# Performance work log

Hardware: AMD Instinct MI355X
Metric: run time of the kernel (lower is better)

## Reference

```python
import jax, jax.numpy as jnp
import numpy as np

B, C, H, W = 8, 128, 64, 64
C8, C2 = C // 8, C // 2


def conv1x1(x, w, b):
    # x: [B,Cin,H,W], w: [Cout,Cin], b: [Cout]
    return jnp.einsum('bchw,oc->bohw', x, w) + b[None, :, None, None]


def maxpool2(x):
    # 2x2 stride-2 max pool on [B,C,H,W]
    b, c, h, w = x.shape
    return x.reshape(b, c, h // 2, 2, w // 2, 2).max(axis=(3, 5))


def setup_inputs() -> dict:
    key = jax.random.key(0)
    ks = jax.random.split(key, 10)
    s_in = 1.0 / np.sqrt(C)
    s_c2 = 1.0 / np.sqrt(C2)
    return {
        'x': jax.random.normal(ks[0], (B, C, H, W), dtype=jnp.float32),
        'w_theta': jax.random.uniform(ks[1], (C8, C), jnp.float32, -s_in, s_in),
        'b_theta': jax.random.uniform(ks[2], (C8,), jnp.float32, -s_in, s_in),
        'w_phi': jax.random.uniform(ks[3], (C8, C), jnp.float32, -s_in, s_in),
        'b_phi': jax.random.uniform(ks[4], (C8,), jnp.float32, -s_in, s_in),
        'w_g': jax.random.uniform(ks[5], (C2, C), jnp.float32, -s_in, s_in),
        'b_g': jax.random.uniform(ks[6], (C2,), jnp.float32, -s_in, s_in),
        'w_attn': jax.random.uniform(ks[7], (C, C2), jnp.float32, -s_c2, s_c2),
        'b_attn': jax.random.uniform(ks[8], (C,), jnp.float32, -s_c2, s_c2),
        'sigma': jnp.zeros((1,), dtype=jnp.float32),
    }


def reference(x, w_theta, b_theta, w_phi, b_phi, w_g, b_g, w_attn, b_attn, sigma):
    b, ch, h, w = x.shape
    n, m = h * w, (h * w) // 4
    theta = conv1x1(x, w_theta, b_theta).reshape(b, ch // 8, n)          # [B,C8,N]
    phi = maxpool2(conv1x1(x, w_phi, b_phi)).reshape(b, ch // 8, m)      # [B,C8,M]
    attn = jax.nn.softmax(jnp.einsum('bdn,bdm->bnm', theta, phi), axis=-1)  # [B,N,M]
    g = maxpool2(conv1x1(x, w_g, b_g)).reshape(b, ch // 2, m)            # [B,C2,M]
    attn_g = jnp.einsum('bcm,bnm->bcn', g, attn).reshape(b, ch // 2, h, w)
    attn_g = conv1x1(attn_g, w_attn, b_attn)
    return x + sigma[0] * attn_g
```

## Files before the change

kernel.cpp:

```cpp
#include <hip/hip_runtime.h>
#include <math.h>

#define Bn 8
#define Cn 128
#define Nn 4096
#define Mn 1024
#define C8n 16
#define C2n 64

typedef __attribute__((ext_vector_type(8))) short short8;
typedef __attribute__((ext_vector_type(4))) float floatx4;
typedef __attribute__((ext_vector_type(4))) unsigned short ushortx4;

__device__ __forceinline__ unsigned short f2bf(float f) {
    union { float f; unsigned u; } v; v.f = f;
    unsigned r = v.u + 0x7fff + ((v.u >> 16) & 1);
    return (unsigned short)(r >> 16);
}

__global__ __launch_bounds__(256) void k1_pre(
    const float* __restrict__ x,
    const float* __restrict__ w_theta, const float* __restrict__ b_theta,
    const float* __restrict__ w_phi,   const float* __restrict__ b_phi,
    const float* __restrict__ w_g,     const float* __restrict__ b_g,
    unsigned short* __restrict__ thA,
    unsigned short* __restrict__ phB,
    unsigned short* __restrict__ gB)
{
    __shared__ unsigned short wA[6 * 4 * 64 * 8];
    __shared__ unsigned short xB[8 * 4 * 64 * 8];
    __shared__ unsigned short pool[80][33];
    __shared__ float biases[96];

    const int t    = threadIdx.x;
    const int b    = blockIdx.x & 7;
    const int h2   = blockIdx.x >> 3;
    const int wv   = t >> 6;
    const int lane = t & 63;
    const int q    = lane >> 4;
    const int l15  = lane & 15;
    const float L2E = 1.4426950408889634f;

    if (t < 96)
        biases[t] = (t < 16) ? b_theta[t] * L2E
                  : (t < 32) ? b_phi[t - 16] : b_g[t - 32];

    #pragma unroll
    for (int k = 0; k < 12; ++k) {
        int u  = t + k * 256;
        int oc = u >> 5, c4 = u & 31;
        const float* src = (oc < 16) ? (w_theta + oc * Cn)
                         : (oc < 32) ? (w_phi + (oc - 16) * Cn)
                                     : (w_g + (oc - 32) * Cn);
        float4 wv4 = *(const float4*)(src + c4 * 4);
        float sc = (oc < 16) ? L2E : 1.f;
        int c = c4 * 4;
        int ot = oc >> 4, kc = c >> 5, qq = (c >> 3) & 3, jj = c & 7;
        ushortx4 pk = { f2bf(wv4.x * sc), f2bf(wv4.y * sc),
                        f2bf(wv4.z * sc), f2bf(wv4.w * sc) };
        *(ushortx4*)(wA + (((ot * 4 + kc) * 64 + qq * 16 + (oc & 15)) * 8 + jj)) = pk;
    }

    const float* xb = x + (size_t)b * Cn * Nn + h2 * 128;
    #pragma unroll
    for (int k = 0; k < 16; ++k) {
        int u   = t + k * 256;
        int pos = u & 127, c4 = u >> 7;
        int c   = c4 * 4;
        float v0 = xb[(size_t)(c + 0) * Nn + pos];
        float v1 = xb[(size_t)(c + 1) * Nn + pos];
        float v2 = xb[(size_t)(c + 2) * Nn + pos];
        float v3 = xb[(size_t)(c + 3) * Nn + pos];
        int pt = pos >> 4, kc = c >> 5, qq = (c >> 3) & 3, jj = c & 7;
        ushortx4 pk = { f2bf(v0), f2bf(v1), f2bf(v2), f2bf(v3) };
        *(ushortx4*)(xB + (((pt * 4 + kc) * 64 + qq * 16 + (pos & 15)) * 8 + jj)) = pk;
    }
    __syncthreads();

    floatx4 acc[6][2];
    #pragma unroll
    for (int ot = 0; ot < 6; ++ot)
        #pragma unroll
        for (int p2 = 0; p2 < 2; ++p2) acc[ot][p2] = (floatx4){0.f, 0.f, 0.f, 0.f};

    #pragma unroll
    for (int kc = 0; kc < 4; ++kc) {
        short8 Bf0 = *(const short8*)(xB + ((wv * 4 + kc) * 64 + lane) * 8);
        short8 Bf1 = *(const short8*)(xB + (((wv + 4) * 4 + kc) * 64 + lane) * 8);
        #pragma unroll
        for (int ot = 0; ot < 6; ++ot) {
            short8 Af = *(const short8*)(wA + ((ot * 4 + kc) * 64 + lane) * 8);
            acc[ot][0] = __builtin_amdgcn_mfma_f32_16x16x32_bf16(Af, Bf0, acc[ot][0], 0, 0, 0);
            acc[ot][1] = __builtin_amdgcn_mfma_f32_16x16x32_bf16(Af, Bf1, acc[ot][1], 0, 0, 0);
        }
    }

    #pragma unroll
    for (int p2 = 0; p2 < 2; ++p2) {
        const int pt = wv + p2 * 4;
        ushortx4 pk;
        #pragma unroll
        for (int r = 0; r < 4; ++r)
            pk[r] = f2bf(acc[0][p2][r] + biases[q * 4 + r]);
        *(ushortx4*)(thA + ((((size_t)b * 256 + h2 * 8 + pt) * 2 + (q >> 1)) * 128
                            + l15 * 8 + (q & 1) * 4)) = pk;
    }

    #pragma unroll
    for (int ot = 1; ot < 6; ++ot) {
        #pragma unroll
        for (int r = 0; r < 4; ++r) {
            float vmax = fmaxf(acc[ot][0][r], acc[ot][1][r]);
            float pmax = fmaxf(vmax, __shfl_xor(vmax, 1, 64));
            if ((l15 & 1) == 0) {
                int oc = (ot - 1) * 16 + q * 4 + r;
                int w2 = wv * 8 + (l15 >> 1);
                pool[oc][w2] = f2bf(pmax + biases[16 + oc]);
            }
        }
    }
    __syncthreads();

    if (t < 64) {
        int w2h = t >> 5, ml = (t >> 1) & 15, dh = t & 1;
        int w2 = w2h * 16 + ml;
        ushortx4 lo, hi;
        #pragma unroll
        for (int j = 0; j < 4; ++j) { lo[j] = pool[dh * 8 + j][w2];
                                      hi[j] = pool[dh * 8 + 4 + j][w2]; }
        unsigned short* dst = phB + (((size_t)b * 64 + h2 * 2 + w2h) * 2 + dh) * 128 + ml * 8;
        *(ushortx4*)dst = lo;
        *(ushortx4*)(dst + 4) = hi;
    }
    {
        int c = t >> 2, sq = t & 3;
        ushortx4 lo, hi;
        #pragma unroll
        for (int j = 0; j < 8; ++j) {
            int w2 = (j & 1) * 16 + sq * 4 + (j >> 1);
            unsigned short v = pool[16 + c][w2];
            if (j < 4) lo[j] = v; else hi[j - 4] = v;
        }
        unsigned short* dst = gB + ((((size_t)b * 32 + h2) * 4 + (c >> 4)) * 4 + sq) * 128
                              + (c & 15) * 8;
        *(ushortx4*)dst = lo;
        *(ushortx4*)(dst + 4) = hi;
    }
}

__global__ __launch_bounds__(256, 2) void k2_attn(
    const float* __restrict__ x,
    const unsigned short* __restrict__ thA,
    const unsigned short* __restrict__ phB,
    const unsigned short* __restrict__ gB,
    const float* __restrict__ w_attn, const float* __restrict__ b_attn,
    const float* __restrict__ sigma_p,
    float* __restrict__ out)
{
    __shared__ float smem[18816];
    unsigned short* phis = (unsigned short*)smem;
    unsigned short* gs   = (unsigned short*)smem + 4096;
    char* Pall = (char*)smem + 40960;
    float* battn = (float*)((char*)smem + 74752);

    const int tid  = threadIdx.x;
    const int wave = tid >> 6;
    const int lane = tid & 63;
    const int q    = lane >> 4;
    const int l15  = lane & 15;
    const int b    = blockIdx.x & 7;
    const int n0   = (blockIdx.x >> 3) * 64;
    const int nw   = n0 + wave * 16;
    char* Pbase = Pall + wave * 8448;

    const float sg = sigma_p[0];

    short8 thf = {};
    if (q < 2)
        thf = *(const short8*)(thA + ((((size_t)b * 256 + (nw >> 4)) * 2 + q) * 16 + l15) * 8);

    floatx4 O[4];
    #pragma unroll
    for (int cs = 0; cs < 4; ++cs) O[cs] = (floatx4){0.f, 0.f, 0.f, 0.f};
    float L[4]    = {0.f, 0.f, 0.f, 0.f};
    float rmax[4] = {-1e30f, -1e30f, -1e30f, -1e30f};

    for (int s = 0; s < 4; ++s) {
        __syncthreads();
        {
            const float4* psrc = (const float4*)(phB + ((size_t)b * 64 + s * 16) * 256);
            const float4* gsrc = (const float4*)(gB + ((size_t)b * 32 + s * 8) * 2048);
            #pragma unroll
            for (int k = 0; k < 10; ++k) {
                int i = tid + k * 256;
                if (i < 512) ((float4*)smem)[i] = psrc[i];
                else ((float4*)((char*)smem + 8192))[i - 512] = gsrc[i - 512];
            }
        }
        __syncthreads();

        floatx4 S[16];
        #pragma unroll
        for (int mt = 0; mt < 16; ++mt) {
            short8 bf = {};
            if (q < 2) bf = *(const short8*)(phis + ((mt * 2 + q) * 16 + l15) * 8);
            S[mt] = __builtin_amdgcn_mfma_f32_16x16x32_bf16(
                        thf, bf, (floatx4){0.f, 0.f, 0.f, 0.f}, 0, 0, 0);
        }

        float cm[4];
        #pragma unroll
        for (int r = 0; r < 4; ++r) cm[r] = S[0][r];
        #pragma unroll
        for (int mt = 1; mt < 16; ++mt)
            #pragma unroll
            for (int r = 0; r < 4; ++r) cm[r] = fmaxf(cm[r], S[mt][r]);
        #pragma unroll
        for (int d = 1; d <= 8; d <<= 1)
            #pragma unroll
            for (int r = 0; r < 4; ++r) cm[r] = fmaxf(cm[r], __shfl_xor(cm[r], d, 64));
        float f[4];
        #pragma unroll
        for (int r = 0; r < 4; ++r) {
            float nm = fmaxf(rmax[r], cm[r]);
            f[r] = exp2f(rmax[r] - nm);
            rmax[r] = nm;
            L[r] *= f[r];
        }
        #pragma unroll
        for (int cs = 0; cs < 4; ++cs)
            #pragma unroll
            for (int r = 0; r < 4; ++r) O[cs][r] *= f[r];

        #pragma unroll
        for (int g2 = 0; g2 < 8; ++g2) {
            #pragma unroll
            for (int r = 0; r < 4; ++r) {
                float pa = exp2f(S[2 * g2][r]     - rmax[r]);
                float pb = exp2f(S[2 * g2 + 1][r] - rmax[r]);
                L[r] += pa + pb;
                unsigned dw = (unsigned)f2bf(pa) | ((unsigned)f2bf(pb) << 16);
                *(unsigned*)(Pbase + (q * 4 + r) * 528 + g2 * 64 + l15 * 4) = dw;
            }
        }
        __syncthreads();

        #pragma unroll
        for (int ch = 0; ch < 8; ++ch) {
            short8 Af = *(const short8*)(Pbase + l15 * 528 + ch * 64 + q * 16);
            const unsigned short* gchunk = gs + ch * 2048;
            #pragma unroll
            for (int cs = 0; cs < 4; ++cs) {
                short8 Bf = *(const short8*)(gchunk + ((cs * 4 + q) * 16 + l15) * 8);
                O[cs] = __builtin_amdgcn_mfma_f32_16x16x32_bf16(Af, Bf, O[cs], 0, 0, 0);
            }
        }
    }

    __syncthreads();
    {
        unsigned short* wAe = (unsigned short*)smem;
        #pragma unroll
        for (int k = 0; k < 8; ++k) {
            int i = tid + k * 256;
            float4 wv = ((const float4*)w_attn)[i];
            int o = i >> 4, c4 = (i & 15) * 4;
            float vv[4] = {wv.x, wv.y, wv.z, wv.w};
            #pragma unroll
            for (int j = 0; j < 4; ++j) {
                int c = c4 + j;
                wAe[((o >> 4) * 2 + (c >> 5)) * 512 + (o & 15) * 32 + (c & 31)] = f2bf(vv[j]);
            }
        }
        if (tid < 128) battn[tid] = b_attn[tid];
    }
    {
        float inv[4];
        #pragma unroll
        for (int r = 0; r < 4; ++r) inv[r] = 1.0f / L[r];
        unsigned short* Ob = (unsigned short*)Pbase;
        #pragma unroll
        for (int cs = 0; cs < 4; ++cs)
            #pragma unroll
            for (int r = 0; r < 4; ++r)
                Ob[(q * 4 + r) * 72 + cs * 16 + l15] = f2bf(O[cs][r] * inv[r]);
    }
    __syncthreads();

    {
        unsigned short* wAe = (unsigned short*)smem;
        unsigned short* Ob = (unsigned short*)Pbase;
        short8 B0 = *(const short8*)(Ob + l15 * 72 + q * 8);
        short8 B1 = *(const short8*)(Ob + l15 * 72 + 32 + q * 8);
        const float* xw = x   + (size_t)b * Cn * Nn + nw + l15;
        float*       ow = out + (size_t)b * Cn * Nn + nw + l15;
        #pragma unroll
        for (int ot = 0; ot < 8; ++ot) {
            short8 A0 = *(const short8*)(wAe + (ot * 2 + 0) * 512 + l15 * 32 + q * 8);
            short8 A1 = *(const short8*)(wAe + (ot * 2 + 1) * 512 + l15 * 32 + q * 8);
            floatx4 D = __builtin_amdgcn_mfma_f32_16x16x32_bf16(
                            A0, B0, (floatx4){0.f, 0.f, 0.f, 0.f}, 0, 0, 0);
            D = __builtin_amdgcn_mfma_f32_16x16x32_bf16(A1, B1, D, 0, 0, 0);
            #pragma unroll
            for (int r = 0; r < 4; ++r) {
                int o = ot * 16 + q * 4 + r;
                float v = D[r] + battn[o];
                ow[(size_t)o * Nn] = xw[(size_t)o * Nn] + sg * v;
            }
        }
    }
}

extern "C" void kernel_launch(void* const* d_in, const int* in_sizes, int n_in,
                              void* d_out, int out_size, void* d_ws, size_t ws_size,
                              hipStream_t stream) {
    const float* x       = (const float*)d_in[0];
    const float* w_theta = (const float*)d_in[1];
    const float* b_theta = (const float*)d_in[2];
    const float* w_phi   = (const float*)d_in[3];
    const float* b_phi   = (const float*)d_in[4];
    const float* w_g     = (const float*)d_in[5];
    const float* b_g     = (const float*)d_in[6];
    const float* w_attn  = (const float*)d_in[7];
    const float* b_attn  = (const float*)d_in[8];
    const float* sigma   = (const float*)d_in[9];
    float* out = (float*)d_out;

    unsigned short* thA = (unsigned short*)d_ws;
    unsigned short* phB = thA + 524288;
    unsigned short* gBp = phB + 131072;

    k1_pre<<<256, 256, 0, stream>>>(x, w_theta, b_theta, w_phi, b_phi,
                                    w_g, b_g, thA, phB, gBp);
    k2_attn<<<512, 256, 0, stream>>>(x, thA, phB, gBp, w_attn, b_attn, sigma, out);
}
```

Before: 117.1 us.

## Register-prefetch next phi/g stage, drop a barrier, use packed bf16 conversion

The attention kernel now loads the next stage's phi and g tiles into registers while the current stage computes, so global-load latency overlaps with the MFMA work. It also removes the barrier between writing P and reading it, which relies on each wave touching only its own P region. In addition, manual bf16 rounding is replaced with the packed __float22bfloat162_rn conversion in several places, and the w_attn transpose now uses vector stores. The prefetch costs 40 extra VGPRs per thread, which may reduce occupancy.

```diff
diff --git a/kernel.cpp b/kernel.cpp
--- a/kernel.cpp
+++ b/kernel.cpp
@@ -1,5 +1,7 @@
 #include <hip/hip_runtime.h>
+#include <hip/hip_bf16.h>
 #include <math.h>
+#include <string.h>
 
 #define Bn 8
 #define Cn 128
@@ -16,6 +18,12 @@
     union { float f; unsigned u; } v; v.f = f;
     unsigned r = v.u + 0x7fff + ((v.u >> 16) & 1);
     return (unsigned short)(r >> 16);
+}
+__device__ __forceinline__ unsigned pk2(float a, float b) {
+    __hip_bfloat162 h = __float22bfloat162_rn(make_float2(a, b));
+    union { __hip_bfloat162 h2; unsigned u; } cv;
+    cv.h2 = h;
+    return cv.u;
 }
 
 __global__ __launch_bounds__(256) void k1_pre(
@@ -56,9 +64,8 @@
         float sc = (oc < 16) ? L2E : 1.f;
         int c = c4 * 4;
         int ot = oc >> 4, kc = c >> 5, qq = (c >> 3) & 3, jj = c & 7;
-        ushortx4 pk = { f2bf(wv4.x * sc), f2bf(wv4.y * sc),
-                        f2bf(wv4.z * sc), f2bf(wv4.w * sc) };
-        *(ushortx4*)(wA + (((ot * 4 + kc) * 64 + qq * 16 + (oc & 15)) * 8 + jj)) = pk;
+        uint2 pk = { pk2(wv4.x * sc, wv4.y * sc), pk2(wv4.z * sc, wv4.w * sc) };
+        *(uint2*)(wA + (((ot * 4 + kc) * 64 + qq * 16 + (oc & 15)) * 8 + jj)) = pk;
     }
 
     const float* xb = x + (size_t)b * Cn * Nn + h2 * 128;
@@ -72,8 +79,8 @@
         float v2 = xb[(size_t)(c + 2) * Nn + pos];
         float v3 = xb[(size_t)(c + 3) * Nn + pos];
         int pt = pos >> 4, kc = c >> 5, qq = (c >> 3) & 3, jj = c & 7;
-        ushortx4 pk = { f2bf(v0), f2bf(v1), f2bf(v2), f2bf(v3) };
-        *(ushortx4*)(xB + (((pt * 4 + kc) * 64 + qq * 16 + (pos & 15)) * 8 + jj)) = pk;
+        uint2 pk = { pk2(v0, v1), pk2(v2, v3) };
+        *(uint2*)(xB + (((pt * 4 + kc) * 64 + qq * 16 + (pos & 15)) * 8 + jj)) = pk;
     }
     __syncthreads();
 
@@ -98,12 +105,13 @@
     #pragma unroll
     for (int p2 = 0; p2 < 2; ++p2) {
         const int pt = wv + p2 * 4;
-        ushortx4 pk;
-        #pragma unroll
-        for (int r = 0; r < 4; ++r)
-            pk[r] = f2bf(acc[0][p2][r] + biases[q * 4 + r]);
-        *(ushortx4*)(thA + ((((size_t)b * 256 + h2 * 8 + pt) * 2 + (q >> 1)) * 128
-                            + l15 * 8 + (q & 1) * 4)) = pk;
+        float v0 = acc[0][p2][0] + biases[q * 4 + 0];
+        float v1 = acc[0][p2][1] + biases[q * 4 + 1];
+        float v2 = acc[0][p2][2] + biases[q * 4 + 2];
+        float v3 = acc[0][p2][3] + biases[q * 4 + 3];
+        uint2 pk = { pk2(v0, v1), pk2(v2, v3) };
+        *(uint2*)(thA + ((((size_t)b * 256 + h2 * 8 + pt) * 2 + (q >> 1)) * 128
+                         + l15 * 8 + (q & 1) * 4)) = pk;
     }
 
     #pragma unroll
@@ -185,19 +193,33 @@
     float L[4]    = {0.f, 0.f, 0.f, 0.f};
     float rmax[4] = {-1e30f, -1e30f, -1e30f, -1e30f};
 
+    const float4* phib = (const float4*)(phB + (size_t)b * 64 * 256);
+    const float4* gbb  = (const float4*)(gB + (size_t)b * 32 * 2048);
+
+    float4 pre[10];
+    #pragma unroll
+    for (int k = 0; k < 10; ++k) {
+        int i = tid + k * 256;
+        pre[k] = (i < 512) ? phib[i] : gbb[i - 512];
+    }
+
     for (int s = 0; s < 4; ++s) {
         __syncthreads();
-        {
-            const float4* psrc = (const float4*)(phB + ((size_t)b * 64 + s * 16) * 256);
-            const float4* gsrc = (const float4*)(gB + ((size_t)b * 32 + s * 8) * 2048);
+        #pragma unroll
+        for (int k = 0; k < 10; ++k) {
+            int i = tid + k * 256;
+            if (i < 512) ((float4*)smem)[i] = pre[k];
+            else ((float4*)((char*)smem + 8192))[i - 512] = pre[k];
+        }
+        __syncthreads();
+        if (s < 3) {
             #pragma unroll
             for (int k = 0; k < 10; ++k) {
                 int i = tid + k * 256;
-                if (i < 512) ((float4*)smem)[i] = psrc[i];
-                else ((float4*)((char*)smem + 8192))[i - 512] = gsrc[i - 512];
-            }
-        }
-        __syncthreads();
+                pre[k] = (i < 512) ? phib[(s + 1) * 512 + i]
+                                   : gbb[(s + 1) * 2048 + (i - 512)];
+            }
+        }
 
         floatx4 S[16];
         #pragma unroll
@@ -239,11 +261,9 @@
                 float pa = exp2f(S[2 * g2][r]     - rmax[r]);
                 float pb = exp2f(S[2 * g2 + 1][r] - rmax[r]);
                 L[r] += pa + pb;
-                unsigned dw = (unsigned)f2bf(pa) | ((unsigned)f2bf(pb) << 16);
-                *(unsigned*)(Pbase + (q * 4 + r) * 528 + g2 * 64 + l15 * 4) = dw;
-            }
-        }
-        __syncthreads();
+                *(unsigned*)(Pbase + (q * 4 + r) * 528 + g2 * 64 + l15 * 4) = pk2(pa, pb);
+            }
+        }
 
         #pragma unroll
         for (int ch = 0; ch < 8; ++ch) {
@@ -264,13 +284,9 @@
         for (int k = 0; k < 8; ++k) {
             int i = tid + k * 256;
             float4 wv = ((const float4*)w_attn)[i];
-            int o = i >> 4, c4 = (i & 15) * 4;
-            float vv[4] = {wv.x, wv.y, wv.z, wv.w};
-            #pragma unroll
-            for (int j = 0; j < 4; ++j) {
-                int c = c4 + j;
-                wAe[((o >> 4) * 2 + (c >> 5)) * 512 + (o & 15) * 32 + (c & 31)] = f2bf(vv[j]);
-            }
+            int o = i >> 4, c = (i & 15) * 4;
+            uint2 pk = { pk2(wv.x, wv.y), pk2(wv.z, wv.w) };
+            *(uint2*)(wAe + ((o >> 4) * 2 + (c >> 5)) * 512 + (o & 15) * 32 + (c & 31)) = pk;
         }
         if (tid < 128) battn[tid] = b_attn[tid];
     }
```

After: 130.9 us. 1.12x slower.
